# Kernel tuning notes

Hardware: AMD Instinct MI355X
Metric: run time of the kernel (lower is better)

The kernel has to match this reference:

```python
import jax, jax.numpy as jnp
import numpy as np

B, T, D, U = 128, 512, 128, 512


def setup_inputs() -> dict:
    key = jax.random.key(0)
    kx, kwx, kwh = jax.random.split(key, 3)
    x = jax.random.normal(kx, (B, T, D), dtype=jnp.float32)
    Wx = jax.random.normal(kwx, (D, U), dtype=jnp.float32) * (1.0 / np.sqrt(D))
    Wh = jax.random.normal(kwh, (U, U), dtype=jnp.float32) * (1.0 / np.sqrt(U))
    b = jnp.zeros((U,), dtype=jnp.float32)
    return {"x": x, "Wx": Wx, "Wh": Wh, "b": b}


def reference(x, Wx, Wh, b):
    # Elman RNN: h_t = tanh(x_t @ Wx + h_{t-1} @ Wh + b)
    # Faithful to MyRNN(return_sequences=True): TensorArray.stack() -> [T, B, U]
    h0 = jnp.zeros((x.shape[0], Wh.shape[0]), dtype=x.dtype)  # fallback zero initial state
    xs = jnp.swapaxes(x, 0, 1)  # [T, B, D] for scan over time

    def step(h, x_t):
        h_new = jnp.tanh(x_t @ Wx + h @ Wh + b)
        return h_new, h_new

    _, seq = jax.lax.scan(step, h0, xs)
    return seq  # [T, B, U]
```

## Files before the change

### kernel.cpp

```cpp
#include <hip/hip_runtime.h>
#include <stddef.h>
#include <stdint.h>


constexpr int B = 128;
constexpr int T = 512;
constexpr int D = 128;
constexpr int U = 512;

typedef _Float16 f16;
typedef _Float16 f16x2 __attribute__((ext_vector_type(2)));
typedef _Float16 f16x8 __attribute__((ext_vector_type(8)));
typedef __fp16   fp16x2 __attribute__((ext_vector_type(2)));
typedef float    f32x4 __attribute__((ext_vector_type(4)));
typedef unsigned int u32;

union U32H2 { u32 u; f16x2 h; fp16x2 p; };

static __device__ __forceinline__ u32 pk(float a, float b) {
    U32H2 c; c.p = __builtin_amdgcn_cvt_pkrtz(a, b); return c.u;
}

#if __has_builtin(__builtin_amdgcn_fdot2)
static __device__ __forceinline__ float fdot2(u32 a, u32 b, float c) {
    U32H2 x, y; x.u = a; y.u = b;
    return __builtin_amdgcn_fdot2(x.h, y.h, c, false);
}
#else
static __device__ __forceinline__ float fdot2(u32 a, u32 b, float c) {
    U32H2 x, y; x.u = a; y.u = b;
    return c + (float)x.h.x * (float)y.h.x + (float)x.h.y * (float)y.h.y;
}
#endif

static __device__ __forceinline__ float fast_tanh(float x) {
    float e = __expf(2.0f * x);
    return 1.0f - 2.0f * __builtin_amdgcn_rcpf(e + 1.0f);
}

__global__ __launch_bounds__(256) void pgemm_kernel(
    const float* __restrict__ x,
    const float* __restrict__ Wx,
    const float* __restrict__ bias,
    float* __restrict__ P)
{
    __shared__ u32 xs[128][66];
    __shared__ u32 ws[64][132];

    const int rb  = blockIdx.x;
    const int cb  = blockIdx.y;
    const int tid = threadIdx.x;
    const int tr  = tid >> 4;
    const int tcc = tid & 15;

    const float4* x4 = (const float4*)x;
#pragma unroll
    for (int l = 0; l < 16; ++l) {
        int idx = tid + l * 256;
        int r   = idx >> 5;
        int q   = idx & 31;
        int m   = rb * 128 + r;
        int b_  = m & 127;
        int t_  = m >> 7;
        float4 v = x4[((size_t)b_ * T + t_) * 32 + q];
        xs[r][2 * q]     = pk(v.x, v.y);
        xs[r][2 * q + 1] = pk(v.z, v.w);
    }
    const float4* W4 = (const float4*)Wx;
#pragma unroll
    for (int l = 0; l < 8; ++l) {
        int idx = tid + l * 256;
        int kp  = idx >> 5;
        int q   = idx & 31;
        float4 a = W4[(size_t)(2 * kp)     * 128 + cb * 32 + q];
        float4 c = W4[(size_t)(2 * kp + 1) * 128 + cb * 32 + q];
        uint4 w;
        w.x = pk(a.x, c.x); w.y = pk(a.y, c.y);
        w.z = pk(a.z, c.z); w.w = pk(a.w, c.w);
        *(uint4*)&ws[kp][4 * q] = w;
    }
    __syncthreads();

    float acc[8][8];
#pragma unroll
    for (int i = 0; i < 8; ++i)
#pragma unroll
        for (int j = 0; j < 8; ++j) acc[i][j] = 0.f;

#pragma unroll 2
    for (int kp = 0; kp < 64; ++kp) {
        u32 xv[8], wv[8];
#pragma unroll
        for (int i = 0; i < 8; ++i) xv[i] = xs[tr + 16 * i][kp];
#pragma unroll
        for (int j = 0; j < 8; ++j) wv[j] = ws[kp][tcc + 16 * j];
#pragma unroll
        for (int i = 0; i < 8; ++i)
#pragma unroll
            for (int j = 0; j < 8; ++j)
                acc[i][j] = fdot2(xv[i], wv[j], acc[i][j]);
    }

#pragma unroll
    for (int j = 0; j < 8; ++j) {
        int c    = cb * 128 + tcc + 16 * j;
        float bv = bias[c];
#pragma unroll
        for (int i = 0; i < 8; ++i) {
            int m = rb * 128 + tr + 16 * i;
            P[(size_t)m * U + c] = acc[i][j] + bv;
        }
    }
}

__global__ __launch_bounds__(512, 2) void rnn_kernel(
    const float* __restrict__ Wh,
    float* __restrict__ out)
{
    __shared__ __align__(16) u32 WL[32768];
    __shared__ __align__(16) u32 hbuf[2][256];

    const int tid = threadIdx.x;
    const int w   = tid >> 6;
    const int l   = tid & 63;
    const int lg  = l >> 4;
    const int lc  = l & 15;
    const int b   = blockIdx.x;

    f16x8 Wf[4][12];
#pragma unroll
    for (int ct = 0; ct < 4; ++ct) {
#pragma unroll
        for (int s = 0; s < 12; ++s) {
            const float* src = Wh + (size_t)(32 * s + 8 * lg) * U
                             + 64 * w + 16 * ct + lc;
            f16x8 f;
#pragma unroll
            for (int e = 0; e < 8; ++e) f[e] = (f16)src[(size_t)e * U];
            Wf[ct][s] = f;
        }
    }
#pragma unroll
    for (int ct = 0; ct < 4; ++ct)
#pragma unroll
        for (int s = 0; s < 12; ++s)
            asm("" : "+v"(Wf[ct][s]));

#pragma unroll
    for (int sr = 0; sr < 4; ++sr) {
#pragma unroll
        for (int ct = 0; ct < 4; ++ct) {
            const float* src = Wh + (size_t)(32 * (12 + sr) + 8 * lg) * U
                             + 64 * w + 16 * ct + lc;
            f16x8 f;
#pragma unroll
            for (int e = 0; e < 8; ++e) f[e] = (f16)src[(size_t)e * U];
            *(f16x8*)&WL[((w * 16 + sr * 4 + ct) * 64 + l) * 4] = f;
        }
    }

    if (tid < 256) { hbuf[0][tid] = 0u; hbuf[1][tid] = 0u; }
    __syncthreads();

    float* outb = out + (size_t)b * U;

    float pv0 = 0.f, pv1 = 0.f, pv2 = 0.f, pv3 = 0.f;
    if (l < 16) {
        pv0 = outb[64 * w + 0  + lc];
        pv1 = outb[64 * w + 16 + lc];
        pv2 = outb[64 * w + 32 + lc];
        pv3 = outb[64 * w + 48 + lc];
    }

    for (int t = 0; t < T; ++t) {
        const int par = t & 1;
        const f16* hb = (const f16*)hbuf[par];

        f32x4 acc0 = (f32x4)0.f, acc1 = (f32x4)0.f;
        f32x4 acc2 = (f32x4)0.f, acc3 = (f32x4)0.f;

#define ALOAD(s) (*(const f16x8*)&hb[32 * (s) + 8 * lg])
#define WLREAD(fi) (*(const f16x8*)&WL[((w * 16 + (fi)) * 64 + l) * 4])

#pragma unroll
        for (int g = 0; g < 4; ++g) {
            f16x8 b0 = WLREAD(4 * g + 0);
            f16x8 b1 = WLREAD(4 * g + 1);
            f16x8 b2 = WLREAD(4 * g + 2);
            f16x8 b3 = WLREAD(4 * g + 3);
#pragma unroll
            for (int s = 3 * g; s < 3 * g + 3; ++s) {
                f16x8 a = ALOAD(s);
                acc0 = __builtin_amdgcn_mfma_f32_16x16x32_f16(a, Wf[0][s], acc0, 0, 0, 0);
                acc1 = __builtin_amdgcn_mfma_f32_16x16x32_f16(a, Wf[1][s], acc1, 0, 0, 0);
                acc2 = __builtin_amdgcn_mfma_f32_16x16x32_f16(a, Wf[2][s], acc2, 0, 0, 0);
                acc3 = __builtin_amdgcn_mfma_f32_16x16x32_f16(a, Wf[3][s], acc3, 0, 0, 0);
            }
            f16x8 a = ALOAD(12 + g);
            acc0 = __builtin_amdgcn_mfma_f32_16x16x32_f16(a, b0, acc0, 0, 0, 0);
            acc1 = __builtin_amdgcn_mfma_f32_16x16x32_f16(a, b1, acc1, 0, 0, 0);
            acc2 = __builtin_amdgcn_mfma_f32_16x16x32_f16(a, b2, acc2, 0, 0, 0);
            acc3 = __builtin_amdgcn_mfma_f32_16x16x32_f16(a, b3, acc3, 0, 0, 0);
        }
#undef ALOAD
#undef WLREAD

        float nv0 = 0.f, nv1 = 0.f, nv2 = 0.f, nv3 = 0.f;
        if (l < 16) {
            float* prow = outb + (size_t)t * (B * U);
            const float* prown = outb + (size_t)((t + 1 < T) ? t + 1 : t) * (B * U);
            f16* hbn = (f16*)hbuf[par ^ 1];

            float h0 = fast_tanh(pv0 + acc0.x);
            float h1 = fast_tanh(pv1 + acc1.x);
            float h2 = fast_tanh(pv2 + acc2.x);
            float h3 = fast_tanh(pv3 + acc3.x);
            prow[64 * w + 0  + lc] = h0;
            prow[64 * w + 16 + lc] = h1;
            prow[64 * w + 32 + lc] = h2;
            prow[64 * w + 48 + lc] = h3;
            hbn[64 * w + 0  + lc] = (f16)h0;
            hbn[64 * w + 16 + lc] = (f16)h1;
            hbn[64 * w + 32 + lc] = (f16)h2;
            hbn[64 * w + 48 + lc] = (f16)h3;

            nv0 = prown[64 * w + 0  + lc];
            nv1 = prown[64 * w + 16 + lc];
            nv2 = prown[64 * w + 32 + lc];
            nv3 = prown[64 * w + 48 + lc];
        }

        asm volatile("s_waitcnt lgkmcnt(0)" ::: "memory");
        __builtin_amdgcn_s_barrier();
        __builtin_amdgcn_sched_barrier(0);

        pv0 = nv0; pv1 = nv1; pv2 = nv2; pv3 = nv3;
    }
}

extern "C" void kernel_launch(void* const* d_in, const int* in_sizes, int n_in,
                              void* d_out, int out_size, void* d_ws, size_t ws_size,
                              hipStream_t stream)
{
    (void)d_ws; (void)ws_size; (void)in_sizes; (void)n_in; (void)out_size;
    const float* x    = (const float*)d_in[0];
    const float* Wx   = (const float*)d_in[1];
    const float* Wh   = (const float*)d_in[2];
    const float* bias = (const float*)d_in[3];
    float* out = (float*)d_out;

    pgemm_kernel<<<dim3((T * B) / 128, U / 128), 256, 0, stream>>>(x, Wx, bias, out);
    rnn_kernel<<<B, 512, 0, stream>>>(Wh, out);
}
```

Baseline: 839.6 us.

## Halve RNN block to 4 waves, each computing 128 output columns

```diff
diff --git a/kernel.cpp b/kernel.cpp
--- a/kernel.cpp
+++ b/kernel.cpp
@@ -113,11 +113,11 @@
     }
 }
 
-__global__ __launch_bounds__(512, 2) void rnn_kernel(
+__global__ __launch_bounds__(256, 1) void rnn_kernel(
     const float* __restrict__ Wh,
     float* __restrict__ out)
 {
-    __shared__ __align__(16) u32 WL[32768];
+    __shared__ __align__(16) u32 WL[39936];
     __shared__ __align__(16) u32 hbuf[2][256];
 
     const int tid = threadIdx.x;
@@ -126,36 +126,48 @@
     const int lg  = l >> 4;
     const int lc  = l & 15;
     const int b   = blockIdx.x;
-
-    f16x8 Wf[4][12];
-#pragma unroll
-    for (int ct = 0; ct < 4; ++ct) {
-#pragma unroll
-        for (int s = 0; s < 12; ++s) {
+    const int cb  = 128 * w;
+
+    f16x8 Wf[8][11];
+    f16x8 Wf11;
+#pragma unroll
+    for (int ct = 0; ct < 8; ++ct) {
+#pragma unroll
+        for (int s = 0; s < 11; ++s) {
             const float* src = Wh + (size_t)(32 * s + 8 * lg) * U
-                             + 64 * w + 16 * ct + lc;
+                             + cb + 16 * ct + lc;
             f16x8 f;
 #pragma unroll
             for (int e = 0; e < 8; ++e) f[e] = (f16)src[(size_t)e * U];
             Wf[ct][s] = f;
         }
     }
-#pragma unroll
-    for (int ct = 0; ct < 4; ++ct)
-#pragma unroll
-        for (int s = 0; s < 12; ++s)
+    {
+        const float* src = Wh + (size_t)(32 * 11 + 8 * lg) * U + cb + lc;
+        f16x8 f;
+#pragma unroll
+        for (int e = 0; e < 8; ++e) f[e] = (f16)src[(size_t)e * U];
+        Wf11 = f;
+    }
+#pragma unroll
+    for (int ct = 0; ct < 8; ++ct)
+#pragma unroll
+        for (int s = 0; s < 11; ++s)
             asm("" : "+v"(Wf[ct][s]));
-
-#pragma unroll
-    for (int sr = 0; sr < 4; ++sr) {
-#pragma unroll
-        for (int ct = 0; ct < 4; ++ct) {
-            const float* src = Wh + (size_t)(32 * (12 + sr) + 8 * lg) * U
-                             + 64 * w + 16 * ct + lc;
+    asm("" : "+v"(Wf11));
+
+#pragma unroll
+    for (int s = 11; s < 16; ++s) {
+#pragma unroll
+        for (int ct = 0; ct < 8; ++ct) {
+            if (s == 11 && ct == 0) continue;
+            int idx = (s - 11) * 8 + ct - 1;
+            const float* src = Wh + (size_t)(32 * s + 8 * lg) * U
+                             + cb + 16 * ct + lc;
             f16x8 f;
 #pragma unroll
             for (int e = 0; e < 8; ++e) f[e] = (f16)src[(size_t)e * U];
-            *(f16x8*)&WL[((w * 16 + sr * 4 + ct) * 64 + l) * 4] = f;
+            *(f16x8*)&WL[((w * 39 + idx) * 64 + l) * 4] = f;
         }
     }
 
@@ -164,77 +176,104 @@
 
     float* outb = out + (size_t)b * U;
 
-    float pv0 = 0.f, pv1 = 0.f, pv2 = 0.f, pv3 = 0.f;
+    float pv[8];
+#pragma unroll
+    for (int ct = 0; ct < 8; ++ct) pv[ct] = 0.f;
     if (l < 16) {
-        pv0 = outb[64 * w + 0  + lc];
-        pv1 = outb[64 * w + 16 + lc];
-        pv2 = outb[64 * w + 32 + lc];
-        pv3 = outb[64 * w + 48 + lc];
+#pragma unroll
+        for (int ct = 0; ct < 8; ++ct) pv[ct] = outb[cb + 16 * ct + lc];
     }
 
     for (int t = 0; t < T; ++t) {
         const int par = t & 1;
         const f16* hb = (const f16*)hbuf[par];
 
-        f32x4 acc0 = (f32x4)0.f, acc1 = (f32x4)0.f;
-        f32x4 acc2 = (f32x4)0.f, acc3 = (f32x4)0.f;
+        f32x4 acc[8];
+#pragma unroll
+        for (int ct = 0; ct < 8; ++ct) acc[ct] = (f32x4)0.f;
 
 #define ALOAD(s) (*(const f16x8*)&hb[32 * (s) + 8 * lg])
-#define WLREAD(fi) (*(const f16x8*)&WL[((w * 16 + (fi)) * 64 + l) * 4])
-
-#pragma unroll
-        for (int g = 0; g < 4; ++g) {
-            f16x8 b0 = WLREAD(4 * g + 0);
-            f16x8 b1 = WLREAD(4 * g + 1);
-            f16x8 b2 = WLREAD(4 * g + 2);
-            f16x8 b3 = WLREAD(4 * g + 3);
-#pragma unroll
-            for (int s = 3 * g; s < 3 * g + 3; ++s) {
-                f16x8 a = ALOAD(s);
-                acc0 = __builtin_amdgcn_mfma_f32_16x16x32_f16(a, Wf[0][s], acc0, 0, 0, 0);
-                acc1 = __builtin_amdgcn_mfma_f32_16x16x32_f16(a, Wf[1][s], acc1, 0, 0, 0);
-                acc2 = __builtin_amdgcn_mfma_f32_16x16x32_f16(a, Wf[2][s], acc2, 0, 0, 0);
-                acc3 = __builtin_amdgcn_mfma_f32_16x16x32_f16(a, Wf[3][s], acc3, 0, 0, 0);
-            }
-            f16x8 a = ALOAD(12 + g);
-            acc0 = __builtin_amdgcn_mfma_f32_16x16x32_f16(a, b0, acc0, 0, 0, 0);
-            acc1 = __builtin_amdgcn_mfma_f32_16x16x32_f16(a, b1, acc1, 0, 0, 0);
-            acc2 = __builtin_amdgcn_mfma_f32_16x16x32_f16(a, b2, acc2, 0, 0, 0);
-            acc3 = __builtin_amdgcn_mfma_f32_16x16x32_f16(a, b3, acc3, 0, 0, 0);
-        }
+#define WLREAD(j) (*(const f16x8*)&WL[((w * 39 + (j)) * 64 + l) * 4])
+#define MM(ct, a, bb) acc[ct] = __builtin_amdgcn_mfma_f32_16x16x32_f16((a), (bb), acc[ct], 0, 0, 0)
+#define REGSLAB(s)                                                        \
+        {                                                                 \
+            f16x8 a_ = ALOAD(s);                                          \
+            MM(0, a_, Wf[0][s]); MM(1, a_, Wf[1][s]);                     \
+            MM(2, a_, Wf[2][s]); MM(3, a_, Wf[3][s]);                     \
+            MM(4, a_, Wf[4][s]); MM(5, a_, Wf[5][s]);                     \
+            MM(6, a_, Wf[6][s]); MM(7, a_, Wf[7][s]);                     \
+        }
+
+        f16x8 sg0, sg1, sg2, sg3, sg4, sg5, sg6, sg7;
+
+        sg0 = WLREAD(0); sg1 = WLREAD(1); sg2 = WLREAD(2); sg3 = WLREAD(3);
+        sg4 = WLREAD(4); sg5 = WLREAD(5); sg6 = WLREAD(6);
+        REGSLAB(0) REGSLAB(1)
+        {
+            f16x8 a_ = ALOAD(11);
+            MM(0, a_, Wf11);
+            MM(1, a_, sg0); MM(2, a_, sg1); MM(3, a_, sg2); MM(4, a_, sg3);
+            MM(5, a_, sg4); MM(6, a_, sg5); MM(7, a_, sg6);
+        }
+        sg0 = WLREAD(7);  sg1 = WLREAD(8);  sg2 = WLREAD(9);  sg3 = WLREAD(10);
+        sg4 = WLREAD(11); sg5 = WLREAD(12); sg6 = WLREAD(13); sg7 = WLREAD(14);
+        REGSLAB(2) REGSLAB(3)
+        {
+            f16x8 a_ = ALOAD(12);
+            MM(0, a_, sg0); MM(1, a_, sg1); MM(2, a_, sg2); MM(3, a_, sg3);
+            MM(4, a_, sg4); MM(5, a_, sg5); MM(6, a_, sg6); MM(7, a_, sg7);
+        }
+        sg0 = WLREAD(15); sg1 = WLREAD(16); sg2 = WLREAD(17); sg3 = WLREAD(18);
+        sg4 = WLREAD(19); sg5 = WLREAD(20); sg6 = WLREAD(21); sg7 = WLREAD(22);
+        REGSLAB(4) REGSLAB(5)
+        {
+            f16x8 a_ = ALOAD(13);
+            MM(0, a_, sg0); MM(1, a_, sg1); MM(2, a_, sg2); MM(3, a_, sg3);
+            MM(4, a_, sg4); MM(5, a_, sg5); MM(6, a_, sg6); MM(7, a_, sg7);
+        }
+        sg0 = WLREAD(23); sg1 = WLREAD(24); sg2 = WLREAD(25); sg3 = WLREAD(26);
+        sg4 = WLREAD(27); sg5 = WLREAD(28); sg6 = WLREAD(29); sg7 = WLREAD(30);
+        REGSLAB(6) REGSLAB(7)
+        {
+            f16x8 a_ = ALOAD(14);
+            MM(0, a_, sg0); MM(1, a_, sg1); MM(2, a_, sg2); MM(3, a_, sg3);
+            MM(4, a_, sg4); MM(5, a_, sg5); MM(6, a_, sg6); MM(7, a_, sg7);
+        }
+        sg0 = WLREAD(31); sg1 = WLREAD(32); sg2 = WLREAD(33); sg3 = WLREAD(34);
+        sg4 = WLREAD(35); sg5 = WLREAD(36); sg6 = WLREAD(37); sg7 = WLREAD(38);
+        REGSLAB(8) REGSLAB(9) REGSLAB(10)
+        {
+            f16x8 a_ = ALOAD(15);
+            MM(0, a_, sg0); MM(1, a_, sg1); MM(2, a_, sg2); MM(3, a_, sg3);
+            MM(4, a_, sg4); MM(5, a_, sg5); MM(6, a_, sg6); MM(7, a_, sg7);
+        }
+#undef REGSLAB
+#undef MM
+#undef WLREAD
 #undef ALOAD
-#undef WLREAD
-
-        float nv0 = 0.f, nv1 = 0.f, nv2 = 0.f, nv3 = 0.f;
+
+        float nv[8];
+#pragma unroll
+        for (int ct = 0; ct < 8; ++ct) nv[ct] = 0.f;
         if (l < 16) {
             float* prow = outb + (size_t)t * (B * U);
             const float* prown = outb + (size_t)((t + 1 < T) ? t + 1 : t) * (B * U);
             f16* hbn = (f16*)hbuf[par ^ 1];
-
-            float h0 = fast_tanh(pv0 + acc0.x);
-            float h1 = fast_tanh(pv1 + acc1.x);
-            float h2 = fast_tanh(pv2 + acc2.x);
-            float h3 = fast_tanh(pv3 + acc3.x);
-            prow[64 * w + 0  + lc] = h0;
-            prow[64 * w + 16 + lc] = h1;
-            prow[64 * w + 32 + lc] = h2;
-            prow[64 * w + 48 + lc] = h3;
-            hbn[64 * w + 0  + lc] = (f16)h0;
-            hbn[64 * w + 16 + lc] = (f16)h1;
-            hbn[64 * w + 32 + lc] = (f16)h2;
-            hbn[64 * w + 48 + lc] = (f16)h3;
-
-            nv0 = prown[64 * w + 0  + lc];
-            nv1 = prown[64 * w + 16 + lc];
-            nv2 = prown[64 * w + 32 + lc];
-            nv3 = prown[64 * w + 48 + lc];
+#pragma unroll
+            for (int ct = 0; ct < 8; ++ct) {
+                float h = fast_tanh(pv[ct] + acc[ct][0]);
+                prow[cb + 16 * ct + lc] = h;
+                hbn[cb + 16 * ct + lc] = (f16)h;
+                nv[ct] = prown[cb + 16 * ct + lc];
+            }
         }
 
         asm volatile("s_waitcnt lgkmcnt(0)" ::: "memory");
         __builtin_amdgcn_s_barrier();
         __builtin_amdgcn_sched_barrier(0);
 
-        pv0 = nv0; pv1 = nv1; pv2 = nv2; pv3 = nv3;
+#pragma unroll
+        for (int ct = 0; ct < 8; ++ct) pv[ct] = nv[ct];
     }
 }
 
@@ -250,5 +289,5 @@
     float* out = (float*)d_out;
 
     pgemm_kernel<<<dim3((T * B) / 128, U / 128), 256, 0, stream>>>(x, Wx, bias, out);
-    rnn_kernel<<<B, 512, 0, stream>>>(Wh, out);
-}
+    rnn_kernel<<<B, 256, 0, stream>>>(Wh, out);
+}
```

New measurement: 1.459 ms. +73.7%, slower.
